# Kernel tuning notes

Measured on AMD Instinct MI355X. Metric: run time of the kernel, lower is better.

Reference implementation:

```python
import jax, jax.numpy as jnp
import numpy as np


def _rgcn(x, src, dst, et, basis, comp, root, bias):
    # Basis-decomposed RGCNConv (PyG semantics): per-relation mean aggregation
    # over incoming edges + root transform + bias.
    N = x.shape[0]
    R = comp.shape[0]
    W = jnp.einsum('rb,bio->rio', comp, basis)          # [R, in, out]
    xr = jnp.einsum('ni,rio->rno', x, W)                 # [R, N, out]
    msg = xr[et, src]                                    # [E, out] gather per edge
    seg = dst * R + et                                   # (target, relation) segment id
    cnt = jax.ops.segment_sum(jnp.ones(et.shape, x.dtype), seg, num_segments=N * R)
    norm = 1.0 / jnp.maximum(cnt, 1.0)                   # mean per (dst, relation)
    msg = msg * norm[seg][:, None]
    agg = jax.ops.segment_sum(msg, dst, num_segments=N)  # scatter-add to targets
    return agg + x @ root + bias


def setup_inputs() -> dict:
    key = jax.random.key(0)
    ks = jax.random.split(key, 20)
    N, E, R, B, F, D, C, NB = 100000, 1600000, 5, 512, 4, 32, 5, 2
    s = 0.1
    inp = {
        'x': jax.random.normal(ks[0], (N, F), jnp.float32),
        'edge_index': jax.random.randint(ks[1], (2, E), 0, N, dtype=jnp.int32),
        'edge_type': jax.random.randint(ks[2], (E,), 0, R, dtype=jnp.int32),
        'start_nodes': jax.random.randint(ks[3], (B,), 0, N, dtype=jnp.int32),
        # layer 0: in=F, out=D
        'basis0': jax.random.normal(ks[4], (NB, F, D), jnp.float32) * s,
        'comp0': jax.random.normal(ks[5], (R, NB), jnp.float32) * s,
        'root0': jax.random.normal(ks[6], (F, D), jnp.float32) * s,
        'bias0': jax.random.normal(ks[7], (D,), jnp.float32) * s,
        # layers 1..3: in=out=D, stacked
        'basis': jax.random.normal(ks[8], (3, NB, D, D), jnp.float32) * s,
        'comp': jax.random.normal(ks[9], (3, R, NB), jnp.float32) * s,
        'root': jax.random.normal(ks[10], (3, D, D), jnp.float32) * s,
        'bias': jax.random.normal(ks[11], (3, D), jnp.float32) * s,
        # MLP head: sum(latent_dim)=128 -> 128 -> C
        'lin1_w': jax.random.normal(ks[12], (4 * D, 128), jnp.float32) * s,
        'lin1_b': jax.random.normal(ks[13], (128,), jnp.float32) * s,
        'lin2_w': jax.random.normal(ks[14], (128, C), jnp.float32) * s,
        'lin2_b': jax.random.normal(ks[15], (C,), jnp.float32) * s,
    }
    return inp


def reference(x, edge_index, edge_type, start_nodes, basis0, comp0, root0, bias0,
              basis, comp, root, bias, lin1_w, lin1_b, lin2_w, lin2_b):
    src, dst = edge_index[0], edge_index[1]
    h = jnp.tanh(_rgcn(x, src, dst, edge_type, basis0, comp0, root0, bias0))
    states = [h]
    for l in range(basis.shape[0]):
        h = jnp.tanh(_rgcn(h, src, dst, edge_type, basis[l], comp[l], root[l], bias[l]))
        states.append(h)
    concat = jnp.concatenate(states, axis=1)             # [N, 128]
    # Per-graph readout: the walk's degenerate n_walks=1 branch, i.e. the
    # start (user) node's concatenated state (sequential backtracking walk
    # replaced by its deterministic initialization path; eval mode, no dropout).
    acc = concat[start_nodes]                            # [B, 128]
    h1 = jax.nn.relu(acc @ lin1_w + lin1_b)
    logits = h1 @ lin2_w + lin2_b
    return jax.nn.log_softmax(logits, axis=-1)
```

## Files before the change

### kernel.cpp

```cpp
#include <hip/hip_runtime.h>
#include <cstdint>

#define N_NODES 100000
#define N_EDGES 1600000
#define R_REL   5
#define NBASIS  2
#define B_START 512
#define PART_SZ 12500
#define NBUCK   256
#define BUCK_SZ 391
#define EPB     6250
#define STAGE_CAP 7000

__device__ __forceinline__ unsigned short f2bf(float f) {
    unsigned u = __float_as_uint(f);
    unsigned r = (u + 0x7FFF + ((u >> 16) & 1)) >> 16;
    return (unsigned short)r;
}


__global__ __launch_bounds__(256) void k_cntb(
    const int* __restrict__ ei, int* __restrict__ bhist) {
    __shared__ int lh[NBUCK];
    int tid = threadIdx.x;
    lh[tid] = 0;
    __syncthreads();
    int base = blockIdx.x * EPB;
    for (int j = tid; j < EPB; j += 256) {
        int dst = ei[N_EDGES + base + j];
        atomicAdd(&lh[dst / BUCK_SZ], 1);
    }
    __syncthreads();
    bhist[blockIdx.x * NBUCK + tid] = lh[tid];
}

__global__ __launch_bounds__(256) void k_colscan(
    int* __restrict__ bhist, int* __restrict__ colsum) {
    __shared__ int s[256];
    int b = blockIdx.x, i = threadIdx.x;
    int v = bhist[i * NBUCK + b];
    s[i] = v;
    __syncthreads();
    for (int o = 1; o < 256; o <<= 1) {
        int t = (i >= o) ? s[i - o] : 0;
        __syncthreads();
        s[i] += t;
        __syncthreads();
    }
    bhist[i * NBUCK + b] = s[i] - v;
    if (i == 255) colsum[b] = s[255];
}

__global__ __launch_bounds__(256) void k_tiny(
    const int* __restrict__ colsum, int* __restrict__ bbase) {
    __shared__ int s[256];
    int i = threadIdx.x;
    int v = colsum[i];
    s[i] = v;
    __syncthreads();
    for (int o = 1; o < 256; o <<= 1) {
        int t = (i >= o) ? s[i - o] : 0;
        __syncthreads();
        s[i] += t;
        __syncthreads();
    }
    bbase[i] = s[i] - v;
    if (i == 255) bbase[NBUCK] = s[255];
}

__global__ __launch_bounds__(256) void k_scat(
    const int* __restrict__ ei, const int* __restrict__ et,
    const int* __restrict__ bhist, const int* __restrict__ bbase,
    int* __restrict__ arena) {
    __shared__ int lc[NBUCK];
    int tid = threadIdx.x;
    lc[tid] = bhist[blockIdx.x * NBUCK + tid] + bbase[tid];
    __syncthreads();
    int base = blockIdx.x * EPB;
    for (int j = tid; j < EPB; j += 256) {
        int e   = base + j;
        int src = ei[e];
        int dst = ei[N_EDGES + e];
        int t   = et[e];
        int bk  = dst / BUCK_SZ;
        int dl  = dst - bk * BUCK_SZ;
        int pos = atomicAdd(&lc[bk], 1);
        arena[pos] = src | (t << 17) | (dl << 20);
    }
}

__global__ __launch_bounds__(256) void k_build(
    const int* __restrict__ arena, const int* __restrict__ bbase,
    int* __restrict__ off, int* __restrict__ pk_m, float* __restrict__ nv5) {
    __shared__ int deg5[BUCK_SZ * R_REL];
    __shared__ int loff[BUCK_SZ + 1];
    __shared__ int cur[BUCK_SZ];
    __shared__ int stg[STAGE_CAP];
    __shared__ int tsum[256];
    int b = blockIdx.x, tid = threadIdx.x;
    int base = bbase[b], end = bbase[b + 1];
    int count = end - base;
    for (int i = tid; i < BUCK_SZ * R_REL; i += 256) deg5[i] = 0;
    __syncthreads();
    for (int i = tid; i < count; i += 256) {
        int r  = arena[base + i];
        int dl = ((unsigned)r) >> 20;
        int t  = (r >> 17) & 7;
        atomicAdd(&deg5[dl * R_REL + t], 1);
    }
    __syncthreads();
    for (int dl = tid; dl < BUCK_SZ; dl += 256) {
        loff[dl] = deg5[dl * R_REL + 0] + deg5[dl * R_REL + 1] +
                   deg5[dl * R_REL + 2] + deg5[dl * R_REL + 3] +
                   deg5[dl * R_REL + 4];
    }
    __syncthreads();
    int d0 = 2 * tid, d1 = 2 * tid + 1;
    int va = (d0 < BUCK_SZ) ? loff[d0] : 0;
    int vb = (d1 < BUCK_SZ) ? loff[d1] : 0;
    tsum[tid] = va + vb;
    __syncthreads();
    for (int o = 1; o < 256; o <<= 1) {
        int v = (tid >= o) ? tsum[tid - o] : 0;
        __syncthreads();
        tsum[tid] += v;
        __syncthreads();
    }
    int pre = tsum[tid] - (va + vb);
    if (d0 < BUCK_SZ) loff[d0] = pre;
    if (d1 < BUCK_SZ) loff[d1] = pre + va;
    __syncthreads();
    for (int dl = tid; dl < BUCK_SZ; dl += 256) {
        int nn = b * BUCK_SZ + dl;
        if (nn < N_NODES) {
            off[nn] = base + loff[dl];
#pragma unroll
            for (int t = 0; t < R_REL; t++) {
                int c = deg5[dl * R_REL + t];
                nv5[nn * R_REL + t] = 1.0f / (float)(c > 0 ? c : 1);
            }
        }
        cur[dl] = loff[dl];
    }
    if (b == NBUCK - 1 && tid == 0) off[N_NODES] = N_EDGES;
    __syncthreads();
    for (int i = tid; i < count; i += 256) {
        int r  = arena[base + i];
        int dl = ((unsigned)r) >> 20;
        int rk = atomicAdd(&cur[dl], 1);
        if (rk < STAGE_CAP) stg[rk] = r;
    }
    __syncthreads();
    for (int i = tid; i < count; i += 256) {
        int r = stg[i < STAGE_CAP ? i : STAGE_CAP - 1];
        pk_m[base + i] = r & 0xFFFFF;
    }
}


template <int IN>
__global__ __launch_bounds__(256) void k_xform(
    const float* __restrict__ h_in, float* __restrict__ h_io,
    unsigned short* __restrict__ y5, const float* __restrict__ basis,
    const float* __restrict__ root, const float* __restrict__ biasL,
    const float* __restrict__ compL) {
    int tid  = threadIdx.x;
    int lane = tid & 31;
    int sub  = tid >> 5;
    int g    = blockIdx.x * 8 + sub;
    float w0[IN], w1[IN], wr[IN];
#pragma unroll
    for (int i = 0; i < IN; i++) {
        w0[i] = basis[i * 32 + lane];
        w1[i] = basis[IN * 32 + i * 32 + lane];
        wr[i] = root[i * 32 + lane];
    }
    float c0[R_REL], c1[R_REL];
#pragma unroll
    for (int r = 0; r < R_REL; r++) {
        c0[r] = compL[r * NBASIS + 0];
        c1[r] = compL[r * NBASIS + 1];
    }
    float bv = biasL[lane];
    for (int n = g; n < N_NODES; n += 8192) {
        float hn = (lane < IN) ? h_in[n * IN + lane] : 0.f;
        float a0 = 0.f, a1 = 0.f, ar = bv;
#pragma unroll
        for (int i = 0; i < IN; i++) {
            float v = __shfl(hn, i, 32);
            a0 += v * w0[i];
            a1 += v * w1[i];
            ar += v * wr[i];
        }
#pragma unroll
        for (int r = 0; r < R_REL; r++)
            y5[(size_t)r * N_NODES * 32 + n * 32 + lane] = f2bf(c0[r] * a0 + c1[r] * a1);
        h_io[n * 32 + lane] = ar;
    }
}


__global__ __launch_bounds__(256) void k_edge(
    const unsigned short* __restrict__ y5, float* __restrict__ h,
    const int* __restrict__ pk_m, const float* __restrict__ nv5,
    const int* __restrict__ off) {
    int tid  = threadIdx.x;
    int lane = tid & 31;
    int sub  = tid >> 5;
    int part  = blockIdx.x & 7;
    int local = (blockIdx.x >> 3) * 8 + sub;
    if (local >= PART_SZ) return;
    int n = part * PART_SZ + local;

    int slot = lane >> 3;
    int cpos = lane & 7;
    float nvt0 = nv5[n * R_REL + 0];
    float nvt1 = nv5[n * R_REL + 1];
    float nvt2 = nv5[n * R_REL + 2];
    float nvt3 = nv5[n * R_REL + 3];
    float nvt4 = nv5[n * R_REL + 4];

    float a0 = 0.f, a1 = 0.f, a2 = 0.f, a3 = 0.f;
    const uint2* __restrict__ yv = (const uint2*)y5;
    int e0 = off[n], e1 = off[n + 1];
    for (int base = e0; base < e1; base += 32) {
        int idx  = base + lane;
        int m    = (idx < e1) ? pk_m[idx] : 0;
        int kmax = e1 - base;
        if (kmax > 32) kmax = 32;
        int j = 0;
        for (; j + 16 <= kmax; j += 16) {
            uint2 uu[4];
            float vv[4];
#pragma unroll
            for (int q = 0; q < 4; q++) {
                int mq = __shfl(m, j + q * 4 + slot, 32);
                int et = mq >> 17;
                vv[q] = (et == 0) ? nvt0 : (et == 1) ? nvt1 : (et == 2) ? nvt2
                      : (et == 3) ? nvt3 : nvt4;
                unsigned row = (unsigned)et * N_NODES + (mq & 0x1FFFF);
                uu[q] = yv[(size_t)row * 8 + cpos];
            }
#pragma unroll
            for (int q = 0; q < 4; q++) {
                float v = vv[q];
                a0 += v * __uint_as_float(uu[q].x << 16);
                a1 += v * __uint_as_float(uu[q].x & 0xFFFF0000u);
                a2 += v * __uint_as_float(uu[q].y << 16);
                a3 += v * __uint_as_float(uu[q].y & 0xFFFF0000u);
            }
        }
        for (; j < kmax; j += 4) {
            int es = j + slot;
            int mq = __shfl(m, es, 32);
            int et = mq >> 17;
            float v = (et == 0) ? nvt0 : (et == 1) ? nvt1 : (et == 2) ? nvt2
                    : (et == 3) ? nvt3 : nvt4;
            v = (es < kmax) ? v : 0.f;
            unsigned row = (unsigned)et * N_NODES + (mq & 0x1FFFF);
            uint2 u = yv[(size_t)row * 8 + cpos];
            a0 += v * __uint_as_float(u.x << 16);
            a1 += v * __uint_as_float(u.x & 0xFFFF0000u);
            a2 += v * __uint_as_float(u.y << 16);
            a3 += v * __uint_as_float(u.y & 0xFFFF0000u);
        }
    }
    a0 += __shfl_xor(a0, 8, 32);  a0 += __shfl_xor(a0, 16, 32);
    a1 += __shfl_xor(a1, 8, 32);  a1 += __shfl_xor(a1, 16, 32);
    a2 += __shfl_xor(a2, 8, 32);  a2 += __shfl_xor(a2, 16, 32);
    a3 += __shfl_xor(a3, 8, 32);  a3 += __shfl_xor(a3, 16, 32);
    if (lane < 8) {
        float4* h4 = (float4*)h;
        float4 hb = h4[(size_t)n * 8 + cpos];
        float4 o;
        o.x = tanhf(hb.x + a0);
        o.y = tanhf(hb.y + a1);
        o.z = tanhf(hb.z + a2);
        o.w = tanhf(hb.w + a3);
        h4[(size_t)n * 8 + cpos] = o;
    }
}


__global__ void k_save(const float* __restrict__ h, const int* __restrict__ start,
                       float* __restrict__ sav) {
    int t = blockIdx.x * blockDim.x + threadIdx.x;
    if (t < B_START * 32) {
        int b = t >> 5, ln = t & 31;
        sav[t] = h[start[b] * 32 + ln];
    }
}

__global__ __launch_bounds__(128) void k_mlp(
    const float* __restrict__ sav, const float* __restrict__ w1,
    const float* __restrict__ b1, const float* __restrict__ w2,
    const float* __restrict__ b2, float* __restrict__ out) {
    __shared__ float cvec[128];
    __shared__ float hb[128];
    __shared__ float lg[8];
    int b = blockIdx.x, t = threadIdx.x;
    cvec[t] = sav[(t >> 5) * (B_START * 32) + b * 32 + (t & 31)];
    __syncthreads();
    float a = b1[t];
#pragma unroll 8
    for (int k = 0; k < 128; k++) a += cvec[k] * w1[k * 128 + t];
    hb[t] = fmaxf(a, 0.f);
    __syncthreads();
    if (t < 5) {
        float a2 = b2[t];
        for (int k = 0; k < 128; k++) a2 += hb[k] * w2[k * 5 + t];
        lg[t] = a2;
    }
    __syncthreads();
    if (t < 5) {
        float m = lg[0];
        for (int j = 1; j < 5; j++) m = fmaxf(m, lg[j]);
        float s = 0.f;
        for (int j = 0; j < 5; j++) s += expf(lg[j] - m);
        out[b * 5 + t] = lg[t] - m - logf(s);
    }
}


extern "C" void kernel_launch(void* const* d_in, const int* in_sizes, int n_in,
                              void* d_out, int out_size, void* d_ws, size_t ws_size,
                              hipStream_t stream) {
    const float* x      = (const float*)d_in[0];
    const int*   ei     = (const int*)d_in[1];
    const int*   etype  = (const int*)d_in[2];
    const int*   start  = (const int*)d_in[3];
    const float* basis0 = (const float*)d_in[4];
    const float* comp0  = (const float*)d_in[5];
    const float* root0  = (const float*)d_in[6];
    const float* bias0  = (const float*)d_in[7];
    const float* basis  = (const float*)d_in[8];
    const float* comp   = (const float*)d_in[9];
    const float* root   = (const float*)d_in[10];
    const float* bias   = (const float*)d_in[11];
    const float* w1     = (const float*)d_in[12];
    const float* b1     = (const float*)d_in[13];
    const float* w2     = (const float*)d_in[14];
    const float* b2     = (const float*)d_in[15];
    float* out = (float*)d_out;

    char* p = (char*)d_ws;
    auto alloc = [&](size_t bytes) -> void* {
        void* r = (void*)p;
        p += (bytes + 255) & ~(size_t)255;
        return r;
    };
    int*            bhist  = (int*)alloc((size_t)NBUCK * NBUCK * 4);
    int*            colsum = (int*)alloc(NBUCK * 4);
    int*            bbase  = (int*)alloc((NBUCK + 1) * 4);
    int*            arena  = (int*)alloc((size_t)N_EDGES * 4);
    int*            off    = (int*)alloc((N_NODES + 1) * 4);
    int*            pk_m   = (int*)alloc((size_t)N_EDGES * 4);
    float*          nv5    = (float*)alloc((size_t)N_NODES * R_REL * 4);
    float*          h      = (float*)alloc((size_t)N_NODES * 32 * 4);
    unsigned short* y5     = (unsigned short*)alloc((size_t)R_REL * N_NODES * 32 * 2);
    float*          sav    = (float*)alloc(4 * B_START * 32 * 4);

    k_cntb<<<NBUCK, 256, 0, stream>>>(ei, bhist);
    k_colscan<<<NBUCK, 256, 0, stream>>>(bhist, colsum);
    k_tiny<<<1, 256, 0, stream>>>(colsum, bbase);
    k_scat<<<NBUCK, 256, 0, stream>>>(ei, etype, bhist, bbase, arena);
    k_build<<<NBUCK, 256, 0, stream>>>(arena, bbase, off, pk_m, nv5);

    int nbEdge = 8 * ((PART_SZ + 7) / 8);
    k_xform<4><<<1024, 256, 0, stream>>>(x, h, y5, basis0, root0, bias0, comp0);
    k_edge<<<nbEdge, 256, 0, stream>>>(y5, h, pk_m, nv5, off);
    k_save<<<64, 256, 0, stream>>>(h, start, sav);
    for (int l = 0; l < 3; l++) {
        k_xform<32><<<1024, 256, 0, stream>>>(h, h, y5,
                                              basis + (size_t)l * 2048,
                                              root + (size_t)l * 1024,
                                              bias + l * 32,
                                              comp + l * 10);
        k_edge<<<nbEdge, 256, 0, stream>>>(y5, h, pk_m, nv5, off);
        k_save<<<64, 256, 0, stream>>>(h, start, sav + (l + 1) * 16384);
    }

    k_mlp<<<B_START, 128, 0, stream>>>(sav, w1, b1, w2, b2, out);
}
```

Measured before the change: 400.0 us.

## Aggregate raw features per relation, then apply relation weights via MFMA GEMM

Swaps transform-then-gather for gather-then-transform. Edges are now sorted by relation within each destination, and per-node per-relation degrees are packed into one word. The edge kernel gathers 32-wide bf16 node features instead of 5x relation-transformed rows, so the per-layer y5 write and its large gather traffic go away. A bf16 MFMA GEMM then applies the combined relation and root weights, using hi/lo bf16 splitting to keep accuracy. The cost is a new agg buffer of 320 bf16 values per node, extra kernels, and degree counts capped at 63 by the 6-bit packing, which could break correctness at high degree.

```diff
diff --git a/kernel.cpp b/kernel.cpp
--- a/kernel.cpp
+++ b/kernel.cpp
@@ -12,10 +12,16 @@
 #define EPB     6250
 #define STAGE_CAP 7000
 
+typedef __attribute__((ext_vector_type(8))) short short8;
+typedef __attribute__((ext_vector_type(4))) float f32x4;
+
 __device__ __forceinline__ unsigned short f2bf(float f) {
     unsigned u = __float_as_uint(f);
     unsigned r = (u + 0x7FFF + ((u >> 16) & 1)) >> 16;
     return (unsigned short)r;
+}
+__device__ __forceinline__ float bf2f(unsigned short u) {
+    return __uint_as_float(((unsigned)u) << 16);
 }
 
 
@@ -91,10 +97,11 @@
 
 __global__ __launch_bounds__(256) void k_build(
     const int* __restrict__ arena, const int* __restrict__ bbase,
-    int* __restrict__ off, int* __restrict__ pk_m, float* __restrict__ nv5) {
+    int* __restrict__ off, int* __restrict__ pk_m, float* __restrict__ nv5,
+    unsigned* __restrict__ degpk) {
     __shared__ int deg5[BUCK_SZ * R_REL];
     __shared__ int loff[BUCK_SZ + 1];
-    __shared__ int cur[BUCK_SZ];
+    __shared__ int cur5[BUCK_SZ * R_REL];
     __shared__ int stg[STAGE_CAP];
     __shared__ int tsum[256];
     int b = blockIdx.x, tid = threadIdx.x;
@@ -132,78 +139,122 @@
     __syncthreads();
     for (int dl = tid; dl < BUCK_SZ; dl += 256) {
         int nn = b * BUCK_SZ + dl;
+        int run = loff[dl];
+        unsigned dp = 0;
+#pragma unroll
+        for (int t = 0; t < R_REL; t++) {
+            cur5[dl * R_REL + t] = run;
+            int c = deg5[dl * R_REL + t];
+            run += c;
+            int cc = c > 63 ? 63 : c;
+            dp |= ((unsigned)cc) << (6 * t);
+        }
         if (nn < N_NODES) {
-            off[nn] = base + loff[dl];
+            off[nn]   = base + loff[dl];
+            degpk[nn] = dp;
 #pragma unroll
             for (int t = 0; t < R_REL; t++) {
                 int c = deg5[dl * R_REL + t];
                 nv5[nn * R_REL + t] = 1.0f / (float)(c > 0 ? c : 1);
             }
         }
-        cur[dl] = loff[dl];
     }
     if (b == NBUCK - 1 && tid == 0) off[N_NODES] = N_EDGES;
     __syncthreads();
     for (int i = tid; i < count; i += 256) {
         int r  = arena[base + i];
         int dl = ((unsigned)r) >> 20;
-        int rk = atomicAdd(&cur[dl], 1);
+        int t  = (r >> 17) & 7;
+        int rk = atomicAdd(&cur5[dl * R_REL + t], 1);
         if (rk < STAGE_CAP) stg[rk] = r;
     }
     __syncthreads();
     for (int i = tid; i < count; i += 256) {
         int r = stg[i < STAGE_CAP ? i : STAGE_CAP - 1];
-        pk_m[base + i] = r & 0xFFFFF;
-    }
-}
-
-
-template <int IN>
-__global__ __launch_bounds__(256) void k_xform(
-    const float* __restrict__ h_in, float* __restrict__ h_io,
-    unsigned short* __restrict__ y5, const float* __restrict__ basis,
-    const float* __restrict__ root, const float* __restrict__ biasL,
-    const float* __restrict__ compL) {
-    int tid  = threadIdx.x;
-    int lane = tid & 31;
-    int sub  = tid >> 5;
-    int g    = blockIdx.x * 8 + sub;
-    float w0[IN], w1[IN], wr[IN];
-#pragma unroll
-    for (int i = 0; i < IN; i++) {
-        w0[i] = basis[i * 32 + lane];
-        w1[i] = basis[IN * 32 + i * 32 + lane];
-        wr[i] = root[i * 32 + lane];
-    }
-    float c0[R_REL], c1[R_REL];
-#pragma unroll
-    for (int r = 0; r < R_REL; r++) {
-        c0[r] = compL[r * NBASIS + 0];
-        c1[r] = compL[r * NBASIS + 1];
-    }
-    float bv = biasL[lane];
-    for (int n = g; n < N_NODES; n += 8192) {
-        float hn = (lane < IN) ? h_in[n * IN + lane] : 0.f;
-        float a0 = 0.f, a1 = 0.f, ar = bv;
-#pragma unroll
-        for (int i = 0; i < IN; i++) {
-            float v = __shfl(hn, i, 32);
-            a0 += v * w0[i];
-            a1 += v * w1[i];
-            ar += v * wr[i];
-        }
-#pragma unroll
-        for (int r = 0; r < R_REL; r++)
-            y5[(size_t)r * N_NODES * 32 + n * 32 + lane] = f2bf(c0[r] * a0 + c1[r] * a1);
-        h_io[n * 32 + lane] = ar;
-    }
-}
-
-
-__global__ __launch_bounds__(256) void k_edge(
-    const unsigned short* __restrict__ y5, float* __restrict__ h,
-    const int* __restrict__ pk_m, const float* __restrict__ nv5,
-    const int* __restrict__ off) {
+        pk_m[base + i] = r & 0x1FFFF;
+    }
+}
+
+
+__global__ __launch_bounds__(256) void k_wprep(
+    const float* __restrict__ basis, const float* __restrict__ comp,
+    const float* __restrict__ root,  const float* __restrict__ basis0,
+    const float* __restrict__ comp0, const float* __restrict__ root0,
+    unsigned short* __restrict__ wf, unsigned short* __restrict__ wf0) {
+    __shared__ float lw[5120];
+    int tid = threadIdx.x;
+    int l = blockIdx.x;
+    if (l < 3) {
+        for (int idx = tid; idx < 5120; idx += 256) {
+            int r = idx >> 10, rem = idx & 1023, i = rem >> 5, o = rem & 31;
+            lw[idx] = comp[l * 10 + r * 2 + 0] * basis[l * 2048 + i * 32 + o]
+                    + comp[l * 10 + r * 2 + 1] * basis[l * 2048 + 1024 + i * 32 + o];
+        }
+        __syncthreads();
+        for (int idx = tid; idx < 12288; idx += 256) {
+            int j = idx & 7, ln = (idx >> 3) & 63;
+            int s = (idx >> 9) % 12, ot = idx / 6144;
+            int o = ot * 16 + (ln & 15), kk = (ln >> 4) * 8 + j;
+            float val;
+            if (s < 10) val = lw[(s % 5) * 1024 + kk * 32 + o];
+            else        val = root[l * 1024 + kk * 32 + o];
+            unsigned short hi = f2bf(val);
+            unsigned short ov = ((s >= 5 && s < 10) || s == 11)
+                                ? f2bf(val - bf2f(hi)) : hi;
+            wf[l * 12288 + idx] = ov;
+        }
+    } else {
+        for (int idx = tid; idx < 1024; idx += 256) {
+            int k = idx >> 5, o = idx & 31;
+            float val = 0.f;
+            if (k < 20) {
+                int r = k >> 2, i = k & 3;
+                val = comp0[r * 2 + 0] * basis0[i * 32 + o]
+                    + comp0[r * 2 + 1] * basis0[128 + i * 32 + o];
+            } else if (k < 24) val = root0[(k - 20) * 32 + o];
+            lw[idx] = val;
+        }
+        __syncthreads();
+        for (int idx = tid; idx < 2048; idx += 256) {
+            int j = idx & 7, ln = (idx >> 3) & 63;
+            int s = (idx >> 9) & 1, ot = idx >> 10;
+            int o = ot * 16 + (ln & 15), kk = (ln >> 4) * 8 + j;
+            float val = lw[kk * 32 + o];
+            unsigned short hi = f2bf(val);
+            wf0[idx] = s ? f2bf(val - bf2f(hi)) : hi;
+        }
+    }
+}
+
+
+__global__ __launch_bounds__(256) void k_cvt0(
+    const float* __restrict__ x, unsigned short* __restrict__ hb0,
+    unsigned short* __restrict__ a0) {
+    int n = blockIdx.x * 256 + threadIdx.x;
+    if (n >= N_NODES) return;
+    float4 xv = *(const float4*)(x + (size_t)n * 4);
+    unsigned short h0 = f2bf(xv.x), h1 = f2bf(xv.y), h2 = f2bf(xv.z), h3 = f2bf(xv.w);
+    unsigned short l0 = f2bf(xv.x - bf2f(h0)), l1 = f2bf(xv.y - bf2f(h1));
+    unsigned short l2 = f2bf(xv.z - bf2f(h2)), l3 = f2bf(xv.w - bf2f(h3));
+    unsigned long long ph = (unsigned long long)h0 | ((unsigned long long)h1 << 16)
+                          | ((unsigned long long)h2 << 32) | ((unsigned long long)h3 << 48);
+    unsigned long long pl = (unsigned long long)l0 | ((unsigned long long)l1 << 16)
+                          | ((unsigned long long)l2 << 32) | ((unsigned long long)l3 << 48);
+    *(unsigned long long*)(hb0 + (size_t)n * 4) = ph;
+    unsigned short* ar = a0 + (size_t)n * 64;
+    uint4 z = {0u, 0u, 0u, 0u};
+    *(unsigned long long*)(ar + 20) = ph;
+    *(uint4*)(ar + 24) = z;
+    *(unsigned long long*)(ar + 52) = pl;
+    *(uint4*)(ar + 56) = z;
+}
+
+
+template <int IN, int SLOTS, int AROW, int LOOFF>
+__global__ __launch_bounds__(256) void k_gath(
+    const unsigned short* __restrict__ hb, const int* __restrict__ pk_m,
+    const float* __restrict__ nv5, const unsigned* __restrict__ degpk,
+    const int* __restrict__ off, unsigned short* __restrict__ agg) {
     int tid  = threadIdx.x;
     int lane = tid & 31;
     int sub  = tid >> 5;
@@ -211,73 +262,135 @@
     int local = (blockIdx.x >> 3) * 8 + sub;
     if (local >= PART_SZ) return;
     int n = part * PART_SZ + local;
-
-    int slot = lane >> 3;
-    int cpos = lane & 7;
-    float nvt0 = nv5[n * R_REL + 0];
-    float nvt1 = nv5[n * R_REL + 1];
-    float nvt2 = nv5[n * R_REL + 2];
-    float nvt3 = nv5[n * R_REL + 3];
-    float nvt4 = nv5[n * R_REL + 4];
-
-    float a0 = 0.f, a1 = 0.f, a2 = 0.f, a3 = 0.f;
-    const uint2* __restrict__ yv = (const uint2*)y5;
-    int e0 = off[n], e1 = off[n + 1];
-    for (int base = e0; base < e1; base += 32) {
-        int idx  = base + lane;
-        int m    = (idx < e1) ? pk_m[idx] : 0;
-        int kmax = e1 - base;
-        if (kmax > 32) kmax = 32;
-        int j = 0;
-        for (; j + 16 <= kmax; j += 16) {
-            uint2 uu[4];
-            float vv[4];
-#pragma unroll
-            for (int q = 0; q < 4; q++) {
-                int mq = __shfl(m, j + q * 4 + slot, 32);
-                int et = mq >> 17;
-                vv[q] = (et == 0) ? nvt0 : (et == 1) ? nvt1 : (et == 2) ? nvt2
-                      : (et == 3) ? nvt3 : nvt4;
-                unsigned row = (unsigned)et * N_NODES + (mq & 0x1FFFF);
-                uu[q] = yv[(size_t)row * 8 + cpos];
+    int c = lane % IN;
+    int s = lane / IN;
+
+    int e0 = off[n];
+    unsigned dp = degpk[n];
+    int chunkbase = e0;
+    int mreg = (chunkbase + lane < N_EDGES) ? pk_m[chunkbase + lane] : 0;
+    int e = e0;
+#pragma unroll
+    for (int r = 0; r < R_REL; r++) {
+        int cnt = (int)((dp >> (6 * r)) & 63u);
+        float acc = 0.f;
+        if (SLOTS == 1) {
+            for (int kb = 0; kb < cnt; kb += 4) {
+                if (e + kb + 3 >= chunkbase + 32) {
+                    chunkbase = e + kb;
+                    mreg = (chunkbase + lane < N_EDGES) ? pk_m[chunkbase + lane] : 0;
+                }
+#pragma unroll
+                for (int q = 0; q < 4; q++) {
+                    int kq = kb + q;
+                    int mq = __shfl(mreg, e + kq - chunkbase, 32);
+                    unsigned short u = hb[(size_t)mq * IN + c];
+                    float v = bf2f(u);
+                    acc += (kq < cnt) ? v : 0.f;
+                }
             }
-#pragma unroll
-            for (int q = 0; q < 4; q++) {
-                float v = vv[q];
-                a0 += v * __uint_as_float(uu[q].x << 16);
-                a1 += v * __uint_as_float(uu[q].x & 0xFFFF0000u);
-                a2 += v * __uint_as_float(uu[q].y << 16);
-                a3 += v * __uint_as_float(uu[q].y & 0xFFFF0000u);
+        } else {
+            for (int kb = 0; kb < cnt; kb += SLOTS) {
+                if (e + kb + SLOTS - 1 >= chunkbase + 32) {
+                    chunkbase = e + kb;
+                    mreg = (chunkbase + lane < N_EDGES) ? pk_m[chunkbase + lane] : 0;
+                }
+                int kq = kb + s;
+                int mq = __shfl(mreg, e + kq - chunkbase, 32);
+                unsigned short u = hb[(size_t)mq * IN + c];
+                float v = bf2f(u);
+                acc += (kq < cnt) ? v : 0.f;
             }
         }
-        for (; j < kmax; j += 4) {
-            int es = j + slot;
-            int mq = __shfl(m, es, 32);
-            int et = mq >> 17;
-            float v = (et == 0) ? nvt0 : (et == 1) ? nvt1 : (et == 2) ? nvt2
-                    : (et == 3) ? nvt3 : nvt4;
-            v = (es < kmax) ? v : 0.f;
-            unsigned row = (unsigned)et * N_NODES + (mq & 0x1FFFF);
-            uint2 u = yv[(size_t)row * 8 + cpos];
-            a0 += v * __uint_as_float(u.x << 16);
-            a1 += v * __uint_as_float(u.x & 0xFFFF0000u);
-            a2 += v * __uint_as_float(u.y << 16);
-            a3 += v * __uint_as_float(u.y & 0xFFFF0000u);
-        }
-    }
-    a0 += __shfl_xor(a0, 8, 32);  a0 += __shfl_xor(a0, 16, 32);
-    a1 += __shfl_xor(a1, 8, 32);  a1 += __shfl_xor(a1, 16, 32);
-    a2 += __shfl_xor(a2, 8, 32);  a2 += __shfl_xor(a2, 16, 32);
-    a3 += __shfl_xor(a3, 8, 32);  a3 += __shfl_xor(a3, 16, 32);
-    if (lane < 8) {
-        float4* h4 = (float4*)h;
-        float4 hb = h4[(size_t)n * 8 + cpos];
-        float4 o;
-        o.x = tanhf(hb.x + a0);
-        o.y = tanhf(hb.y + a1);
-        o.z = tanhf(hb.z + a2);
-        o.w = tanhf(hb.w + a3);
-        h4[(size_t)n * 8 + cpos] = o;
+        e += cnt;
+        if (SLOTS > 1) {
+            acc += __shfl_xor(acc, 4, 32);
+            acc += __shfl_xor(acc, 8, 32);
+            acc += __shfl_xor(acc, 16, 32);
+        }
+        float sc = acc * nv5[n * R_REL + r];
+        unsigned short hi = f2bf(sc);
+        unsigned short lo = f2bf(sc - bf2f(hi));
+        if (s == 0) {
+            agg[(size_t)n * AROW + r * IN + c] = hi;
+            agg[(size_t)n * AROW + LOOFF + r * IN + c] = lo;
+        }
+    }
+}
+
+
+__global__ __launch_bounds__(256) void k_gemm(
+    const unsigned short* __restrict__ agg, const unsigned short* __restrict__ hbin,
+    const unsigned short* __restrict__ wfl, const float* __restrict__ biasL,
+    float* __restrict__ h, unsigned short* __restrict__ hbout) {
+    int tid = threadIdx.x;
+    int wid = tid >> 6, lane = tid & 63;
+    int tile = blockIdx.x * 4 + wid;
+    if (tile >= N_NODES / 16) return;
+    int n0 = tile * 16;
+    int row = lane & 15, kg = lane >> 4;
+    const short8* ar = (const short8*)(agg + (size_t)(n0 + row) * 320 + kg * 8);
+    const short8* wv = (const short8*)wfl;
+    short8 hbf = *(const short8*)(hbin + (size_t)(n0 + row) * 32 + kg * 8);
+    f32x4 c0 = {0.f, 0.f, 0.f, 0.f}, c1 = {0.f, 0.f, 0.f, 0.f};
+#pragma unroll
+    for (int s = 0; s < 5; s++) {
+        short8 a = ar[s * 4];
+        c0 = __builtin_amdgcn_mfma_f32_16x16x32_bf16(a, wv[s * 64 + lane], c0, 0, 0, 0);
+        c1 = __builtin_amdgcn_mfma_f32_16x16x32_bf16(a, wv[(12 + s) * 64 + lane], c1, 0, 0, 0);
+        c0 = __builtin_amdgcn_mfma_f32_16x16x32_bf16(a, wv[(5 + s) * 64 + lane], c0, 0, 0, 0);
+        c1 = __builtin_amdgcn_mfma_f32_16x16x32_bf16(a, wv[(17 + s) * 64 + lane], c1, 0, 0, 0);
+        short8 al = ar[20 + s * 4];
+        c0 = __builtin_amdgcn_mfma_f32_16x16x32_bf16(al, wv[s * 64 + lane], c0, 0, 0, 0);
+        c1 = __builtin_amdgcn_mfma_f32_16x16x32_bf16(al, wv[(12 + s) * 64 + lane], c1, 0, 0, 0);
+    }
+    c0 = __builtin_amdgcn_mfma_f32_16x16x32_bf16(hbf, wv[10 * 64 + lane], c0, 0, 0, 0);
+    c1 = __builtin_amdgcn_mfma_f32_16x16x32_bf16(hbf, wv[22 * 64 + lane], c1, 0, 0, 0);
+    c0 = __builtin_amdgcn_mfma_f32_16x16x32_bf16(hbf, wv[11 * 64 + lane], c0, 0, 0, 0);
+    c1 = __builtin_amdgcn_mfma_f32_16x16x32_bf16(hbf, wv[23 * 64 + lane], c1, 0, 0, 0);
+    float b0 = biasL[row], b1 = biasL[16 + row];
+#pragma unroll
+    for (int i = 0; i < 4; i++) {
+        int n = n0 + kg * 4 + i;
+        float t0 = tanhf(c0[i] + b0);
+        float t1 = tanhf(c1[i] + b1);
+        h[(size_t)n * 32 + row]      = t0;
+        h[(size_t)n * 32 + 16 + row] = t1;
+        hbout[(size_t)n * 32 + row]      = f2bf(t0);
+        hbout[(size_t)n * 32 + 16 + row] = f2bf(t1);
+    }
+}
+
+__global__ __launch_bounds__(256) void k_gemm0(
+    const unsigned short* __restrict__ a0, const unsigned short* __restrict__ wf0,
+    const float* __restrict__ biasL, float* __restrict__ h,
+    unsigned short* __restrict__ hbout) {
+    int tid = threadIdx.x;
+    int wid = tid >> 6, lane = tid & 63;
+    int tile = blockIdx.x * 4 + wid;
+    if (tile >= N_NODES / 16) return;
+    int n0 = tile * 16;
+    int row = lane & 15, kg = lane >> 4;
+    const short8* ar = (const short8*)(a0 + (size_t)(n0 + row) * 64 + kg * 8);
+    const short8* wv = (const short8*)wf0;
+    short8 a01 = ar[0], a23 = ar[4];
+    f32x4 c0 = {0.f, 0.f, 0.f, 0.f}, c1 = {0.f, 0.f, 0.f, 0.f};
+    c0 = __builtin_amdgcn_mfma_f32_16x16x32_bf16(a01, wv[0 * 64 + lane], c0, 0, 0, 0);
+    c1 = __builtin_amdgcn_mfma_f32_16x16x32_bf16(a01, wv[2 * 64 + lane], c1, 0, 0, 0);
+    c0 = __builtin_amdgcn_mfma_f32_16x16x32_bf16(a01, wv[1 * 64 + lane], c0, 0, 0, 0);
+    c1 = __builtin_amdgcn_mfma_f32_16x16x32_bf16(a01, wv[3 * 64 + lane], c1, 0, 0, 0);
+    c0 = __builtin_amdgcn_mfma_f32_16x16x32_bf16(a23, wv[0 * 64 + lane], c0, 0, 0, 0);
+    c1 = __builtin_amdgcn_mfma_f32_16x16x32_bf16(a23, wv[2 * 64 + lane], c1, 0, 0, 0);
+    float b0 = biasL[row], b1 = biasL[16 + row];
+#pragma unroll
+    for (int i = 0; i < 4; i++) {
+        int n = n0 + kg * 4 + i;
+        float t0 = tanhf(c0[i] + b0);
+        float t1 = tanhf(c1[i] + b1);
+        h[(size_t)n * 32 + row]      = t0;
+        h[(size_t)n * 32 + 16 + row] = t1;
+        hbout[(size_t)n * 32 + row]      = f2bf(t0);
+        hbout[(size_t)n * 32 + 16 + row] = f2bf(t1);
     }
 }
 
@@ -287,7 +400,7 @@
     int t = blockIdx.x * blockDim.x + threadIdx.x;
     if (t < B_START * 32) {
         int b = t >> 5, ln = t & 31;
-        sav[t] = h[start[b] * 32 + ln];
+        sav[t] = h[(size_t)start[b] * 32 + ln];
     }
 }
 
@@ -356,27 +469,33 @@
     int*            off    = (int*)alloc((N_NODES + 1) * 4);
     int*            pk_m   = (int*)alloc((size_t)N_EDGES * 4);
     float*          nv5    = (float*)alloc((size_t)N_NODES * R_REL * 4);
+    unsigned*       degpk  = (unsigned*)alloc((size_t)N_NODES * 4);
     float*          h      = (float*)alloc((size_t)N_NODES * 32 * 4);
-    unsigned short* y5     = (unsigned short*)alloc((size_t)R_REL * N_NODES * 32 * 2);
+    unsigned short* hbuf   = (unsigned short*)alloc((size_t)N_NODES * 32 * 2);
+    unsigned short* hb0    = (unsigned short*)alloc((size_t)N_NODES * 4 * 2);
+    unsigned short* agg    = (unsigned short*)alloc((size_t)N_NODES * 320 * 2);
+    unsigned short* wf     = (unsigned short*)alloc((size_t)3 * 12288 * 2);
+    unsigned short* wf0    = (unsigned short*)alloc((size_t)2048 * 2);
     float*          sav    = (float*)alloc(4 * B_START * 32 * 4);
 
     k_cntb<<<NBUCK, 256, 0, stream>>>(ei, bhist);
     k_colscan<<<NBUCK, 256, 0, stream>>>(bhist, colsum);
     k_tiny<<<1, 256, 0, stream>>>(colsum, bbase);
     k_scat<<<NBUCK, 256, 0, stream>>>(ei, etype, bhist, bbase, arena);
-    k_build<<<NBUCK, 256, 0, stream>>>(arena, bbase, off, pk_m, nv5);
-
-    int nbEdge = 8 * ((PART_SZ + 7) / 8);
-    k_xform<4><<<1024, 256, 0, stream>>>(x, h, y5, basis0, root0, bias0, comp0);
-    k_edge<<<nbEdge, 256, 0, stream>>>(y5, h, pk_m, nv5, off);
+    k_build<<<NBUCK, 256, 0, stream>>>(arena, bbase, off, pk_m, nv5, degpk);
+    k_wprep<<<4, 256, 0, stream>>>(basis, comp, root, basis0, comp0, root0, wf, wf0);
+    k_cvt0<<<(N_NODES + 255) / 256, 256, 0, stream>>>(x, hb0, agg);
+
+    int nbGath = 8 * ((PART_SZ + 7) / 8);
+    int nbGemm = (N_NODES / 16 + 3) / 4;
+
+    k_gath<4, 8, 64, 32><<<nbGath, 256, 0, stream>>>(hb0, pk_m, nv5, degpk, off, agg);
+    k_gemm0<<<nbGemm, 256, 0, stream>>>(agg, wf0, bias0, h, hbuf);
     k_save<<<64, 256, 0, stream>>>(h, start, sav);
     for (int l = 0; l < 3; l++) {
-        k_xform<32><<<1024, 256, 0, stream>>>(h, h, y5,
-                                              basis + (size_t)l * 2048,
-                                              root + (size_t)l * 1024,
-                                              bias + l * 32,
-                                              comp + l * 10);
-        k_edge<<<nbEdge, 256, 0, stream>>>(y5, h, pk_m, nv5, off);
+        k_gath<32, 1, 320, 160><<<nbGath, 256, 0, stream>>>(hbuf, pk_m, nv5, degpk, off, agg);
+        k_gemm<<<nbGemm, 256, 0, stream>>>(agg, hbuf, wf + (size_t)l * 12288,
+                                           bias + l * 32, h, hbuf);
         k_save<<<64, 256, 0, stream>>>(h, start, sav + (l + 1) * 16384);
     }
 
```

Result: slower. 417.8 us (+4.4%).
